# Optimization experiments

Measured on AMD Instinct MI355X. Metric: run time of the kernel, lower is better.

## Reference

```python
import jax, jax.numpy as jnp
import numpy as np

N = 16384      # nodes
DEG = 20       # avg degree
E = N * DEG    # edges
MUL = 8        # multiplicity of 0e and 1o irreps
NB = 10        # number_of_basis
HID = 64       # fc hidden size
RMAX = 3.5     # max_radius
WNUM = 4 * MUL * MUL  # tp weight numel (4 parity-allowed paths)


def setup_inputs() -> dict:
    key = jax.random.key(0)
    ks = jax.random.split(key, 12)
    f = jax.random.normal(ks[0], (N, 4 * MUL), dtype=jnp.float32)  # 8 scalars + 8 vectors (3 comps)
    pos = jax.random.uniform(ks[1], (N, 3), dtype=jnp.float32) * 2.0  # box keeps dists < RMAX
    rng = np.random.default_rng(0)
    edge_dst = np.repeat(np.arange(N), DEG)
    edge_src = rng.integers(0, N, size=E)
    edge_src = np.where(edge_src == edge_dst, (edge_src + 1) % N, edge_src)
    return {
        'f': f, 'pos': pos,
        'Wq_s': jax.random.normal(ks[2], (MUL, MUL), jnp.float32),
        'Wq_v': jax.random.normal(ks[3], (MUL, MUL), jnp.float32),
        'Wk1': jax.random.normal(ks[4], (NB, HID), jnp.float32),
        'Wk2': jax.random.normal(ks[5], (HID, WNUM), jnp.float32),
        'Wv1': jax.random.normal(ks[6], (NB, HID), jnp.float32),
        'Wv2': jax.random.normal(ks[7], (HID, WNUM), jnp.float32),
        'Wd_s': jax.random.normal(ks[8], (MUL, MUL), jnp.float32),
        'Wd_v': jax.random.normal(ks[9], (MUL, MUL), jnp.float32),
        'edge_src': jnp.asarray(edge_src, jnp.int32),
        'edge_dst': jnp.asarray(edge_dst, jnp.int32),
    }


def _soft_unit_step(x):
    # e3nn soft_unit_step: exp(-1/x) for x>0 else 0; safe for grads
    xs = jnp.where(x > 0, x, 1.0)
    return jnp.where(x > 0, jnp.exp(-1.0 / xs), 0.0)


def _split(x):
    # [*, 4*MUL] -> scalars [*, MUL], vectors [*, MUL, 3]
    return x[:, :MUL], x[:, MUL:].reshape(-1, MUL, 3)


def _fc(x, W1, W2):
    # e3nn FullyConnectedNet: normalized linear -> act -> normalized linear
    h = jax.nn.silu(x @ W1 / jnp.sqrt(jnp.float32(NB)))
    return h @ W2 / jnp.sqrt(jnp.float32(HID))


def _tp(xs, xv, s0, s1, w):
    # fully connected tensor product (in: MULx0e+MULx1o) x (1x0e+1x1o) -> MULx0e+MULx1o
    # w: [E, 4, MUL, MUL]; paths: ss->s, vv->s (dot/sqrt3), sv->v, vs->v
    norm = 1.0 / (MUL ** 0.5 * 2.0 ** 0.5)
    out_s = (jnp.einsum('ei,eio->eo', xs * s0[:, None], w[:, 0]) +
             jnp.einsum('eic,ec,eio->eo', xv, s1, w[:, 1]) / 3.0 ** 0.5) * norm
    out_v = (jnp.einsum('ei,ec,eio->eoc', xs, s1, w[:, 2]) +
             jnp.einsum('eic,eio->eoc', xv * s0[:, None, None], w[:, 3])) * norm
    return out_s, out_v


def reference(f, pos, Wq_s, Wq_v, Wk1, Wk2, Wv1, Wv2, Wd_s, Wd_v, edge_src, edge_dst):
    edge_vec = pos[edge_src] - pos[edge_dst]                      # [E,3]
    r = jnp.linalg.norm(edge_vec, axis=1)                         # [E]
    # soft_one_hot_linspace, basis='smooth_finite', cutoff=True
    values = jnp.linspace(0.0, RMAX, NB + 2)[1:-1]
    step = RMAX / (NB + 1)
    d = (r[:, None] - values) / step
    basis = (1.14136 * np.exp(2.0)) * _soft_unit_step(d + 1.0) * _soft_unit_step(1.0 - d)
    emb = basis * NB ** 0.5                                       # [E,NB]
    cutoff = _soft_unit_step(10.0 * (1.0 - r / RMAX))             # [E]
    # spherical harmonics l=0,1; normalize=True, 'component' norm
    unit = edge_vec / r[:, None]
    s0 = jnp.ones_like(r)
    s1 = (3.0 ** 0.5) * unit                                      # [E,3]
    # query (equivariant linear per irrep)
    fs, fv = _split(f)
    qs = fs @ Wq_s / MUL ** 0.5                                   # [N,MUL]
    qv = jnp.einsum('eic,io->eoc', fv, Wq_v) / MUL ** 0.5         # [N,MUL,3]
    # per-edge tp weights from radial net
    wk = _fc(emb, Wk1, Wk2).reshape(E, 4, MUL, MUL)
    wv = _fc(emb, Wv1, Wv2).reshape(E, 4, MUL, MUL)
    gs, gv = fs[edge_src], fv[edge_src]                           # gather
    ks_, kv_ = _tp(gs, gv, s0, s1, wk)
    vs_, vv_ = _tp(gs, gv, s0, s1, wv)
    # dot tp (q x k -> 0e), shared weights
    qds, qdv = qs[edge_dst], qv[edge_dst]
    logits = (jnp.einsum('ei,ej,ij->e', qds, ks_, Wd_s) +
              jnp.einsum('eic,ejc,ij->e', qdv, kv_, Wd_v) / 3.0 ** 0.5) / (MUL * 2.0 ** 0.5)
    # scatter softmax with cutoff weighting
    mx = jax.ops.segment_max(logits, edge_dst, num_segments=N)
    mx = jnp.where(jnp.isneginf(mx), 0.0, mx)
    expw = cutoff * jnp.exp(logits - mx[edge_dst])
    z = jax.ops.segment_sum(expw, edge_dst, num_segments=N)
    z = jnp.where(z == 0, 1.0, z)
    alpha = expw / z[edge_dst]
    coef = jnp.sqrt(jax.nn.relu(alpha) + 1e-12)                   # [E]
    out_s = jax.ops.segment_sum(coef[:, None] * vs_, edge_dst, num_segments=N)
    out_v = jax.ops.segment_sum(coef[:, None, None] * vv_, edge_dst, num_segments=N)
    return jnp.concatenate([out_s, out_v.reshape(N, 3 * MUL)], axis=1)
```

## Files before the change

kernel.cpp:

```cpp
#include <hip/hip_runtime.h>
#include <hip/hip_bf16.h>
#include <math.h>

#define NN 16384
#define DEG 20
#define EE (NN*DEG)
#define RMAXF 3.5f
#define NGRP 5

typedef __attribute__((ext_vector_type(8))) short short8;
typedef __attribute__((ext_vector_type(4))) float f32x4;

__device__ __forceinline__ float su_f(float x) {
    return x > 0.0f ? __expf(-__builtin_amdgcn_rcpf(x)) : 0.0f;
}
__device__ __forceinline__ ushort f2bf(float x) {
    __hip_bfloat16 h = __float2bfloat16(x);
    return *reinterpret_cast<ushort*>(&h);
}

__global__ __launch_bounds__(256, 3) void edge_kernel(
    const float* __restrict__ f,   const float* __restrict__ pos,
    const float* __restrict__ Wqs, const float* __restrict__ Wqv,
    const float* __restrict__ Wds, const float* __restrict__ Wdv,
    const float* __restrict__ Wk1, const float* __restrict__ Wv1,
    const float* __restrict__ Wk2, const float* __restrict__ Wv2,
    const int* __restrict__ esrc,  float* __restrict__ out)
{
    __shared__ float  s_w[2][16][260];
    __shared__ __align__(16) ushort s_hb[2][16][64];
    __shared__ __align__(16) float s_g[16][36];
    __shared__ float s_emb[16][10];
    __shared__ float s_s1[16][4];
    __shared__ float s_b[16][9];
    __shared__ float s_v[80][33];
    __shared__ float s_lg[80];
    __shared__ float s_cut[80];
    __shared__ float s_mqn[4][32];
    __shared__ int   s_esrc[80];

    const int t = threadIdx.x;
    const int wave = t >> 6, lane = t & 63;
    const int qd = lane >> 4, n = lane & 15;
    const int n0 = blockIdx.x * 4;
    const int E0 = n0 * DEG;

    if (t < 128) {
        int nd = t >> 5, idx = t & 31;
        const float* fr = f + (size_t)(n0 + nd) * 32;
        const float inv8 = 0.35355339059327373f;
        float o_ = 0.0f;
        if (idx < 8) {
            int j = idx;
            #pragma unroll
            for (int i = 0; i < 8; i++) {
                float qs = 0.0f;
                #pragma unroll
                for (int a = 0; a < 8; a++) qs = fmaf(fr[a], Wqs[a * 8 + i], qs);
                o_ = fmaf(qs * inv8, Wds[i * 8 + j], o_);
            }
        } else {
            int kk = idx - 8;
            int j = kk / 3, c = kk - 3 * j;
            #pragma unroll
            for (int i = 0; i < 8; i++) {
                float qv = 0.0f;
                #pragma unroll
                for (int a = 0; a < 8; a++) qv = fmaf(fr[8 + 3 * a + c], Wqv[a * 8 + i], qv);
                o_ = fmaf(qv * inv8, Wdv[i * 8 + j], o_);
            }
            o_ *= 0.5773502691896258f;
        }
        s_mqn[nd][idx] = o_;
    }
    if (t < 80) s_esrc[t] = esrc[E0 + t];

    float wk1r[10], wv1r[10];
    #pragma unroll
    for (int j = 0; j < 10; j++) {
        wk1r[j] = Wk1[j * 64 + lane];
        wv1r[j] = Wv1[j * 64 + lane];
    }

    short8 breg[2][2][4];
    #pragma unroll
    for (int net = 0; net < 2; net++) {
        const float* W2 = net ? Wv2 : Wk2;
        #pragma unroll
        for (int s = 0; s < 2; s++)
            #pragma unroll
            for (int jj = 0; jj < 4; jj++) {
                int col = (wave * 4 + jj) * 16 + n;
                union { ushort u[8]; short8 v; } bf;
                #pragma unroll
                for (int j = 0; j < 8; j++) {
                    int k0 = s * 32 + qd * 8 + j;
                    bf.u[j] = f2bf(W2[k0 * 256 + col] * 0.125f);
                }
                breg[net][s][jj] = bf.v;
            }
    }

    __syncthreads();

    for (int g = 0; g < NGRP; g++) {
        const int le0 = g * 16;

        {
            int e = t >> 4, rl = t & 15;
            if (rl < 11) {
                int s = s_esrc[le0 + e];
                int d = n0 + (le0 + e) / DEG;
                float vx = pos[s * 3 + 0] - pos[d * 3 + 0];
                float vy = pos[s * 3 + 1] - pos[d * 3 + 1];
                float vz = pos[s * 3 + 2] - pos[d * 3 + 2];
                float r = sqrtf(vx * vx + vy * vy + vz * vz);
                if (rl < 10) {
                    const float step = RMAXF / 11.0f;
                    const float invstep = 11.0f / RMAXF;
                    const float K = 26.66929988626f;
                    float dd = (r - step * (float)(rl + 1)) * invstep;
                    s_emb[e][rl] = K * su_f(dd + 1.0f) * su_f(1.0f - dd);
                } else {
                    float invr = __builtin_amdgcn_rcpf(r);
                    const float sqrt3 = 1.7320508075688772f;
                    s_s1[e][0] = sqrt3 * vx * invr;
                    s_s1[e][1] = sqrt3 * vy * invr;
                    s_s1[e][2] = sqrt3 * vz * invr;
                    s_cut[le0 + e] = su_f(10.0f * (1.0f - r / RMAXF));
                }
            }
        }
        if (t < 128) {
            int el = t >> 3, c4 = t & 7;
            int s = s_esrc[le0 + el];
            float4 x = *reinterpret_cast<const float4*>(f + (size_t)s * 32 + c4 * 4);
            *reinterpret_cast<float4*>(&s_g[el][c4 * 4]) = x;
        }
        __syncthreads();

        {
            const float invsq10 = 0.31622776601683794f;
            #pragma unroll
            for (int e = 0; e < 4; e++) {
                int el = wave * 4 + e;
                float ak = 0.0f, av = 0.0f;
                #pragma unroll
                for (int j = 0; j < 10; j++) {
                    float ej = s_emb[el][j];
                    ak = fmaf(ej, wk1r[j], ak);
                    av = fmaf(ej, wv1r[j], av);
                }
                ak *= invsq10; av *= invsq10;
                float hk = ak * __builtin_amdgcn_rcpf(1.0f + __expf(-ak));
                float hv = av * __builtin_amdgcn_rcpf(1.0f + __expf(-av));
                int pos_ = ((((lane >> 3) ^ (el & 7))) << 3) | (lane & 7);
                s_hb[0][el][pos_] = f2bf(hk);
                s_hb[1][el][pos_] = f2bf(hv);
            }
            if (t < 128) {
                int el = t >> 3, k = t & 7;
                const float inv_sqrt3 = 0.5773502691896258f;
                s_b[el][k] = (s_g[el][8 + 3 * k + 0] * s_s1[el][0] +
                              s_g[el][8 + 3 * k + 1] * s_s1[el][1] +
                              s_g[el][8 + 3 * k + 2] * s_s1[el][2]) * inv_sqrt3;
            }
        }
        __syncthreads();

        #pragma unroll
        for (int net = 0; net < 2; net++) {
            short8 ha0 = *(const short8*)&s_hb[net][n][((qd ^ (n & 7)) << 3)];
            short8 ha1 = *(const short8*)&s_hb[net][n][(((4 + qd) ^ (n & 7)) << 3)];
            #pragma unroll
            for (int jj = 0; jj < 4; jj++) {
                int tt = wave * 4 + jj;
                f32x4 d = {0.0f, 0.0f, 0.0f, 0.0f};
                d = __builtin_amdgcn_mfma_f32_16x16x32_bf16(ha0, breg[net][0][jj], d, 0, 0, 0);
                d = __builtin_amdgcn_mfma_f32_16x16x32_bf16(ha1, breg[net][1][jj], d, 0, 0, 0);
                #pragma unroll
                for (int r = 0; r < 4; r++)
                    s_w[net][4 * qd + r][tt * 16 + n] = d[r];
            }
        }
        __syncthreads();

        {
            int el = t >> 4, role = t & 15;
            int le = le0 + el;
            int nd = le / DEG;
            float g[32];
            #pragma unroll
            for (int v4 = 0; v4 < 8; v4++) {
                float4 x = *reinterpret_cast<const float4*>(&s_g[el][v4 * 4]);
                g[v4 * 4 + 0] = x.x; g[v4 * 4 + 1] = x.y;
                g[v4 * 4 + 2] = x.z; g[v4 * 4 + 3] = x.w;
            }
            const float nrm = 0.25f;
            const float* wk = s_w[0][el];
            const float* wv = s_w[1][el];
            float contrib = 0.0f;

            if (role < 8) {
                int o = role;
                float ks = 0.0f, vs = 0.0f;
                #pragma unroll
                for (int i = 0; i < 8; i++) {
                    float ai = g[i], bi = s_b[el][i];
                    ks += ai * wk[i * 8 + o] + bi * wk[64 + i * 8 + o];
                    vs += ai * wv[i * 8 + o] + bi * wv[64 + i * 8 + o];
                }
                contrib = s_mqn[nd][o] * (ks * nrm);
                s_v[le][o] = vs * nrm;
            } else {
                int o = role - 8;
                float uk = 0.0f, uv = 0.0f;
                #pragma unroll
                for (int i = 0; i < 8; i++) {
                    uk = fmaf(g[i], wk[128 + i * 8 + o], uk);
                    uv = fmaf(g[i], wv[128 + i * 8 + o], uv);
                }
                #pragma unroll
                for (int c = 0; c < 3; c++) {
                    float tk = 0.0f, tv = 0.0f;
                    #pragma unroll
                    for (int i = 0; i < 8; i++) {
                        float gc = g[8 + 3 * i + c];
                        tk = fmaf(gc, wk[192 + i * 8 + o], tk);
                        tv = fmaf(gc, wv[192 + i * 8 + o], tv);
                    }
                    float s1c = s_s1[el][c];
                    float kv_c = nrm * (s1c * uk + tk);
                    contrib = fmaf(s_mqn[nd][8 + 3 * o + c], kv_c, contrib);
                    s_v[le][8 + o * 3 + c] = nrm * (s1c * uv + tv);
                }
            }
            contrib += __shfl_xor(contrib, 1);
            contrib += __shfl_xor(contrib, 2);
            contrib += __shfl_xor(contrib, 4);
            contrib += __shfl_xor(contrib, 8);
            if (role == 0) s_lg[le] = contrib * 0.08838834764831845f;
        }
        __syncthreads();
    }

    {
        int base_le = DEG * wave;
        int h32 = lane & 32;
        int hl = lane & 31;
        float lg = -INFINITY, cw = 0.0f;
        if (hl < DEG) {
            lg = s_lg[base_le + hl];
            cw = s_cut[base_le + hl];
        }
        float mx = lg;
        mx = fmaxf(mx, __shfl_xor(mx, 16));
        mx = fmaxf(mx, __shfl_xor(mx, 8));
        mx = fmaxf(mx, __shfl_xor(mx, 4));
        mx = fmaxf(mx, __shfl_xor(mx, 2));
        mx = fmaxf(mx, __shfl_xor(mx, 1));

        float ew = cw * __expf(lg - mx);
        float z = ew;
        z += __shfl_xor(z, 16);
        z += __shfl_xor(z, 8);
        z += __shfl_xor(z, 4);
        z += __shfl_xor(z, 2);
        z += __shfl_xor(z, 1);
        z = (z == 0.0f) ? 1.0f : z;
        float coef = sqrtf(ew * __builtin_amdgcn_rcpf(z) + 1e-12f);

        float acc = 0.0f;
        #pragma unroll
        for (int ee = 0; ee < DEG; ee++) {
            float ce = __shfl(coef, h32 + ee);
            acc = fmaf(ce, s_v[base_le + ee][hl], acc);
        }
        if (lane < 32) out[(size_t)(n0 + wave) * 32 + hl] = acc;
    }
}

extern "C" void kernel_launch(void* const* d_in, const int* in_sizes, int n_in,
                              void* d_out, int out_size, void* d_ws, size_t ws_size,
                              hipStream_t stream) {
    const float* f    = (const float*)d_in[0];
    const float* pos  = (const float*)d_in[1];
    const float* Wqs  = (const float*)d_in[2];
    const float* Wqv  = (const float*)d_in[3];
    const float* Wk1  = (const float*)d_in[4];
    const float* Wk2  = (const float*)d_in[5];
    const float* Wv1  = (const float*)d_in[6];
    const float* Wv2  = (const float*)d_in[7];
    const float* Wds  = (const float*)d_in[8];
    const float* Wdv  = (const float*)d_in[9];
    const int* esrc   = (const int*)d_in[10];
    float* out        = (float*)d_out;

    edge_kernel<<<dim3(NN / 4), dim3(256), 0, stream>>>(
        f, pos, Wqs, Wqv, Wds, Wdv, Wk1, Wv1, Wk2, Wv2, esrc, out);
}
```

Baseline: 211.4 us.

## Prefetch next edge group's gathers with double buffering and store values in bf16

```diff
diff --git a/kernel.cpp b/kernel.cpp
--- a/kernel.cpp
+++ b/kernel.cpp
@@ -17,6 +17,9 @@
 __device__ __forceinline__ ushort f2bf(float x) {
     __hip_bfloat16 h = __float2bfloat16(x);
     return *reinterpret_cast<ushort*>(&h);
+}
+__device__ __forceinline__ float bf2f(ushort u) {
+    return __uint_as_float(((unsigned int)u) << 16);
 }
 
 __global__ __launch_bounds__(256, 3) void edge_kernel(
@@ -29,11 +32,11 @@
 {
     __shared__ float  s_w[2][16][260];
     __shared__ __align__(16) ushort s_hb[2][16][64];
-    __shared__ __align__(16) float s_g[16][36];
-    __shared__ float s_emb[16][10];
-    __shared__ float s_s1[16][4];
+    __shared__ __align__(16) float s_g[2][16][36];
+    __shared__ float s_emb[2][16][10];
+    __shared__ float s_s1[2][16][4];
     __shared__ float s_b[16][9];
-    __shared__ float s_v[80][33];
+    __shared__ __align__(4) ushort s_v[80][34];
     __shared__ float s_lg[80];
     __shared__ float s_cut[80];
     __shared__ float s_mqn[4][32];
@@ -74,6 +77,7 @@
         s_mqn[nd][idx] = o_;
     }
     if (t < 80) s_esrc[t] = esrc[E0 + t];
+    __syncthreads();
 
     float wk1r[10], wv1r[10];
     #pragma unroll
@@ -101,69 +105,112 @@
             }
     }
 
+    {
+        int e = t >> 4, rl = t & 15;
+        if (rl < 11) {
+            int s = s_esrc[e];
+            int d = n0;
+            float vx = pos[s * 3 + 0] - pos[d * 3 + 0];
+            float vy = pos[s * 3 + 1] - pos[d * 3 + 1];
+            float vz = pos[s * 3 + 2] - pos[d * 3 + 2];
+            float r = sqrtf(vx * vx + vy * vy + vz * vz);
+            if (rl < 10) {
+                const float step = RMAXF / 11.0f;
+                const float invstep = 11.0f / RMAXF;
+                const float K = 26.66929988626f;
+                float dd = (r - step * (float)(rl + 1)) * invstep;
+                s_emb[0][e][rl] = K * su_f(dd + 1.0f) * su_f(1.0f - dd);
+            } else {
+                float invr = __builtin_amdgcn_rcpf(r);
+                const float sqrt3 = 1.7320508075688772f;
+                s_s1[0][e][0] = sqrt3 * vx * invr;
+                s_s1[0][e][1] = sqrt3 * vy * invr;
+                s_s1[0][e][2] = sqrt3 * vz * invr;
+                s_cut[e] = su_f(10.0f * (1.0f - r / RMAXF));
+            }
+        }
+        if (t < 128) {
+            int el = t >> 3, c4 = t & 7;
+            int s = s_esrc[el];
+            float4 x = *reinterpret_cast<const float4*>(f + (size_t)s * 32 + c4 * 4);
+            *reinterpret_cast<float4*>(&s_g[0][el][c4 * 4]) = x;
+        }
+    }
     __syncthreads();
 
     for (int g = 0; g < NGRP; g++) {
+        const int cb = g & 1, nbuf = cb ^ 1;
         const int le0 = g * 16;
-
+        const bool more = (g + 1 < NGRP);
+
+        float psx = 0.f, psy = 0.f, psz = 0.f, pdx = 0.f, pdy = 0.f, pdz = 0.f;
+        float4 pf4 = {0.f, 0.f, 0.f, 0.f};
         {
             int e = t >> 4, rl = t & 15;
+            if (more && rl < 11) {
+                int s = s_esrc[le0 + 16 + e];
+                int d = n0 + (le0 + 16 + e) / DEG;
+                psx = pos[s * 3 + 0]; psy = pos[s * 3 + 1]; psz = pos[s * 3 + 2];
+                pdx = pos[d * 3 + 0]; pdy = pos[d * 3 + 1]; pdz = pos[d * 3 + 2];
+            }
+            if (more && t < 128) {
+                int el = t >> 3, c4 = t & 7;
+                int s = s_esrc[le0 + 16 + el];
+                pf4 = *reinterpret_cast<const float4*>(f + (size_t)s * 32 + c4 * 4);
+            }
+        }
+
+        {
+            const float invsq10 = 0.31622776601683794f;
+            #pragma unroll
+            for (int e = 0; e < 4; e++) {
+                int el = wave * 4 + e;
+                float ak = 0.0f, av = 0.0f;
+                #pragma unroll
+                for (int j = 0; j < 10; j++) {
+                    float ej = s_emb[cb][el][j];
+                    ak = fmaf(ej, wk1r[j], ak);
+                    av = fmaf(ej, wv1r[j], av);
+                }
+                ak *= invsq10; av *= invsq10;
+                float hk = ak * __builtin_amdgcn_rcpf(1.0f + __expf(-ak));
+                float hv = av * __builtin_amdgcn_rcpf(1.0f + __expf(-av));
+                int pos_ = ((((lane >> 3) ^ (el & 7))) << 3) | (lane & 7);
+                s_hb[0][el][pos_] = f2bf(hk);
+                s_hb[1][el][pos_] = f2bf(hv);
+            }
+            if (t < 128) {
+                int el = t >> 3, k = t & 7;
+                const float inv_sqrt3 = 0.5773502691896258f;
+                s_b[el][k] = (s_g[cb][el][8 + 3 * k + 0] * s_s1[cb][el][0] +
+                              s_g[cb][el][8 + 3 * k + 1] * s_s1[cb][el][1] +
+                              s_g[cb][el][8 + 3 * k + 2] * s_s1[cb][el][2]) * inv_sqrt3;
+            }
+        }
+
+        if (more) {
+            int e = t >> 4, rl = t & 15;
             if (rl < 11) {
-                int s = s_esrc[le0 + e];
-                int d = n0 + (le0 + e) / DEG;
-                float vx = pos[s * 3 + 0] - pos[d * 3 + 0];
-                float vy = pos[s * 3 + 1] - pos[d * 3 + 1];
-                float vz = pos[s * 3 + 2] - pos[d * 3 + 2];
+                float vx = psx - pdx, vy = psy - pdy, vz = psz - pdz;
                 float r = sqrtf(vx * vx + vy * vy + vz * vz);
                 if (rl < 10) {
                     const float step = RMAXF / 11.0f;
                     const float invstep = 11.0f / RMAXF;
                     const float K = 26.66929988626f;
                     float dd = (r - step * (float)(rl + 1)) * invstep;
-                    s_emb[e][rl] = K * su_f(dd + 1.0f) * su_f(1.0f - dd);
+                    s_emb[nbuf][e][rl] = K * su_f(dd + 1.0f) * su_f(1.0f - dd);
                 } else {
                     float invr = __builtin_amdgcn_rcpf(r);
                     const float sqrt3 = 1.7320508075688772f;
-                    s_s1[e][0] = sqrt3 * vx * invr;
-                    s_s1[e][1] = sqrt3 * vy * invr;
-                    s_s1[e][2] = sqrt3 * vz * invr;
-                    s_cut[le0 + e] = su_f(10.0f * (1.0f - r / RMAXF));
-                }
-            }
-        }
-        if (t < 128) {
-            int el = t >> 3, c4 = t & 7;
-            int s = s_esrc[le0 + el];
-            float4 x = *reinterpret_cast<const float4*>(f + (size_t)s * 32 + c4 * 4);
-            *reinterpret_cast<float4*>(&s_g[el][c4 * 4]) = x;
-        }
-        __syncthreads();
-
-        {
-            const float invsq10 = 0.31622776601683794f;
-            #pragma unroll
-            for (int e = 0; e < 4; e++) {
-                int el = wave * 4 + e;
-                float ak = 0.0f, av = 0.0f;
-                #pragma unroll
-                for (int j = 0; j < 10; j++) {
-                    float ej = s_emb[el][j];
-                    ak = fmaf(ej, wk1r[j], ak);
-                    av = fmaf(ej, wv1r[j], av);
-                }
-                ak *= invsq10; av *= invsq10;
-                float hk = ak * __builtin_amdgcn_rcpf(1.0f + __expf(-ak));
-                float hv = av * __builtin_amdgcn_rcpf(1.0f + __expf(-av));
-                int pos_ = ((((lane >> 3) ^ (el & 7))) << 3) | (lane & 7);
-                s_hb[0][el][pos_] = f2bf(hk);
-                s_hb[1][el][pos_] = f2bf(hv);
+                    s_s1[nbuf][e][0] = sqrt3 * vx * invr;
+                    s_s1[nbuf][e][1] = sqrt3 * vy * invr;
+                    s_s1[nbuf][e][2] = sqrt3 * vz * invr;
+                    s_cut[le0 + 16 + e] = su_f(10.0f * (1.0f - r / RMAXF));
+                }
             }
             if (t < 128) {
-                int el = t >> 3, k = t & 7;
-                const float inv_sqrt3 = 0.5773502691896258f;
-                s_b[el][k] = (s_g[el][8 + 3 * k + 0] * s_s1[el][0] +
-                              s_g[el][8 + 3 * k + 1] * s_s1[el][1] +
-                              s_g[el][8 + 3 * k + 2] * s_s1[el][2]) * inv_sqrt3;
+                int el = t >> 3, c4 = t & 7;
+                *reinterpret_cast<float4*>(&s_g[nbuf][el][c4 * 4]) = pf4;
             }
         }
         __syncthreads();
@@ -189,12 +236,12 @@
             int el = t >> 4, role = t & 15;
             int le = le0 + el;
             int nd = le / DEG;
-            float g[32];
+            float g_[32];
             #pragma unroll
             for (int v4 = 0; v4 < 8; v4++) {
-                float4 x = *reinterpret_cast<const float4*>(&s_g[el][v4 * 4]);
-                g[v4 * 4 + 0] = x.x; g[v4 * 4 + 1] = x.y;
-                g[v4 * 4 + 2] = x.z; g[v4 * 4 + 3] = x.w;
+                float4 x = *reinterpret_cast<const float4*>(&s_g[cb][el][v4 * 4]);
+                g_[v4 * 4 + 0] = x.x; g_[v4 * 4 + 1] = x.y;
+                g_[v4 * 4 + 2] = x.z; g_[v4 * 4 + 3] = x.w;
             }
             const float nrm = 0.25f;
             const float* wk = s_w[0][el];
@@ -206,33 +253,33 @@
                 float ks = 0.0f, vs = 0.0f;
                 #pragma unroll
                 for (int i = 0; i < 8; i++) {
-                    float ai = g[i], bi = s_b[el][i];
+                    float ai = g_[i], bi = s_b[el][i];
                     ks += ai * wk[i * 8 + o] + bi * wk[64 + i * 8 + o];
                     vs += ai * wv[i * 8 + o] + bi * wv[64 + i * 8 + o];
                 }
                 contrib = s_mqn[nd][o] * (ks * nrm);
-                s_v[le][o] = vs * nrm;
+                s_v[le][o] = f2bf(vs * nrm);
             } else {
                 int o = role - 8;
                 float uk = 0.0f, uv = 0.0f;
                 #pragma unroll
                 for (int i = 0; i < 8; i++) {
-                    uk = fmaf(g[i], wk[128 + i * 8 + o], uk);
-                    uv = fmaf(g[i], wv[128 + i * 8 + o], uv);
+                    uk = fmaf(g_[i], wk[128 + i * 8 + o], uk);
+                    uv = fmaf(g_[i], wv[128 + i * 8 + o], uv);
                 }
                 #pragma unroll
                 for (int c = 0; c < 3; c++) {
                     float tk = 0.0f, tv = 0.0f;
                     #pragma unroll
                     for (int i = 0; i < 8; i++) {
-                        float gc = g[8 + 3 * i + c];
+                        float gc = g_[8 + 3 * i + c];
                         tk = fmaf(gc, wk[192 + i * 8 + o], tk);
                         tv = fmaf(gc, wv[192 + i * 8 + o], tv);
                     }
-                    float s1c = s_s1[el][c];
+                    float s1c = s_s1[cb][el][c];
                     float kv_c = nrm * (s1c * uk + tk);
                     contrib = fmaf(s_mqn[nd][8 + 3 * o + c], kv_c, contrib);
-                    s_v[le][8 + o * 3 + c] = nrm * (s1c * uv + tv);
+                    s_v[le][8 + o * 3 + c] = f2bf(nrm * (s1c * uv + tv));
                 }
             }
             contrib += __shfl_xor(contrib, 1);
@@ -274,7 +321,7 @@
         #pragma unroll
         for (int ee = 0; ee < DEG; ee++) {
             float ce = __shfl(coef, h32 + ee);
-            acc = fmaf(ce, s_v[base_le + ee][hl], acc);
+            acc = fmaf(ce, bf2f(s_v[base_le + ee][hl]), acc);
         }
         if (lane < 32) out[(size_t)(n0 + wave) * 32 + hl] = acc;
     }
```

New measurement: 208.0 us. About the same (-1.6%).
